# Kernel tuning notes

Measured on AMD Instinct MI355X. Metric: run time of the kernel, lower is better.

Reference implementation:

```python
import jax, jax.numpy as jnp
import numpy as np

N = 50000      # nodes
E = 800000     # edges (avg degree 16)
IN, H, OUT = 128, 128, 64


def setup_inputs() -> dict:
    key = jax.random.key(0)
    k1, k2, k3, k4 = jax.random.split(key, 4)
    x = jax.random.normal(k1, (N, IN), dtype=jnp.float32)
    edge_index = jax.random.randint(k2, (2, E), 0, N, dtype=jnp.int32)
    W1 = jax.random.normal(k3, (IN, H), dtype=jnp.float32) * (1.0 / np.sqrt(IN))
    b1 = jnp.zeros((H,), dtype=jnp.float32)
    W2 = jax.random.normal(k4, (H, OUT), dtype=jnp.float32) * (1.0 / np.sqrt(H))
    b2 = jnp.zeros((OUT,), dtype=jnp.float32)
    return {"x": x, "edge_index": edge_index, "W1": W1, "b1": b1, "W2": W2, "b2": b2}


def gcn_conv(x, edge_index, W, b):
    """PyG GCNConv: D^-1/2 (A + I) D^-1/2 (x W) + b, with self-loops."""
    src, dst = edge_index[0], edge_index[1]
    h = x @ W                                              # [N, F_out] transform first (F_out <= F_in path)
    ones = jnp.ones((src.shape[0],), dtype=h.dtype)
    deg = jax.ops.segment_sum(ones, dst, num_segments=N) + 1.0  # +1 for self-loop
    inv_sqrt_deg = jax.lax.rsqrt(deg)
    norm = inv_sqrt_deg[src] * inv_sqrt_deg[dst]           # [E]
    agg = jax.ops.segment_sum(h[src] * norm[:, None], dst, num_segments=N)
    # self-loop contribution: norm_ii = deg_i^-1
    return agg + h * (1.0 / deg)[:, None] + b


def reference(x, edge_index, W1, b1, W2, b2):
    h = jax.nn.relu(gcn_conv(x, edge_index, W1, b1))
    return gcn_conv(h, edge_index, W2, b2)
```

## Files before the change

kernel.cpp:

```cpp
#include <hip/hip_runtime.h>
#include <hip/hip_bf16.h>


#define GCN_IN   128
#define GCN_H    128
#define GCN_OUT  64
#define CAP      64
#define OVF_CAP  65536
#define SCAT_BLOCKS 2048

using short8 = __attribute__((ext_vector_type(8))) short;
using f32x4  = __attribute__((ext_vector_type(4))) float;
using int4v  = __attribute__((ext_vector_type(4))) int;

__device__ __forceinline__ ushort f2bf(float f) {
    uint b = __float_as_uint(f);
    b = (b + 0x7FFFu + ((b >> 16) & 1u)) >> 16;
    return (ushort)b;
}
__device__ __forceinline__ float bf2f_lo(uint u) { return __uint_as_float(u << 16); }
__device__ __forceinline__ float bf2f_hi(uint u) { return __uint_as_float(u & 0xFFFF0000u); }

__global__ __launch_bounds__(256) void k_fused1(
        const int* __restrict__ src, const int* __restrict__ dst,
        int* __restrict__ cnt, ushort* __restrict__ slot,
        int* __restrict__ ovfcnt, int2* __restrict__ ovf, int E,
        const float* __restrict__ A, const float* __restrict__ B,
        ushort* __restrict__ C, int M, int N) {
    __shared__ __align__(16) ushort As[64][40];
    __shared__ __align__(16) ushort Bs[128][40];
    const int tid = threadIdx.x;

    if (blockIdx.x < SCAT_BLOCKS) {
        const int part = blockIdx.x & 7;
        const int psz  = (N + 7) >> 3;
        const int lo   = part * psz;
        const int hi   = min(lo + psz, N);
        const int bip  = blockIdx.x >> 3;
        const int stride4 = (SCAT_BLOCKS >> 3) * 256 * 4;
        for (int e = (bip * 256 + tid) * 4; e < E; e += stride4) {
            int4v d4 = __builtin_nontemporal_load((const int4v*)(dst + e));
            int4v s4 = __builtin_nontemporal_load((const int4v*)(src + e));
            #pragma unroll
            for (int k = 0; k < 4; ++k) {
                int d = d4[k];
                int s = s4[k];
                if (d >= lo && d < hi) {
                    int pos = atomicAdd(&cnt[d], 1);
                    if (pos < CAP) {
                        slot[(size_t)d * CAP + pos] = (ushort)s;
                    } else {
                        int q = atomicAdd(ovfcnt, 1);
                        if (q < OVF_CAP) ovf[q] = make_int2(d, s);
                    }
                }
            }
        }
        return;
    }

    const int g    = blockIdx.x - SCAT_BLOCKS;
    const int row0 = g * 64;
    const int w    = tid >> 6;
    const int lane = tid & 63;
    const int l15  = lane & 15;
    const int q8   = (lane >> 4) * 8;

    f32x4 acc[8];
    #pragma unroll
    for (int t = 0; t < 8; ++t) {
        acc[t][0] = 0.f; acc[t][1] = 0.f; acc[t][2] = 0.f; acc[t][3] = 0.f;
    }
    for (int kb = 0; kb < 128; kb += 32) {
        #pragma unroll
        for (int tt = 0; tt < 2; ++tt) {
            int f = tid * 4 + tt * 1024;
            int r = f >> 5;
            int k = f & 31;
            float4 v = make_float4(0.f, 0.f, 0.f, 0.f);
            int gr = row0 + r;
            if (gr < M) v = *(const float4*)(A + (size_t)gr * 128 + kb + k);
            ushort4 o;
            o.x = f2bf(v.x); o.y = f2bf(v.y); o.z = f2bf(v.z); o.w = f2bf(v.w);
            *(ushort4*)&As[r][k] = o;
        }
        #pragma unroll
        for (int tt = 0; tt < 4; ++tt) {
            int f = tid * 4 + tt * 1024;
            int k = f >> 7;
            int n = f & 127;
            float4 v = *(const float4*)(B + (size_t)(kb + k) * 128 + n);
            Bs[n + 0][k] = f2bf(v.x);
            Bs[n + 1][k] = f2bf(v.y);
            Bs[n + 2][k] = f2bf(v.z);
            Bs[n + 3][k] = f2bf(v.w);
        }
        __syncthreads();
        short8 a = *(const short8*)&As[16 * w + l15][q8];
        #pragma unroll
        for (int t = 0; t < 8; ++t) {
            short8 b = *(const short8*)&Bs[16 * t + l15][q8];
            acc[t] = __builtin_amdgcn_mfma_f32_16x16x32_bf16(a, b, acc[t], 0, 0, 0);
        }
        __syncthreads();
    }
    const int quad = lane >> 4;
    #pragma unroll
    for (int r = 0; r < 4; ++r) {
        int grow = row0 + 16 * w + quad * 4 + r;
        if (grow < M) {
            #pragma unroll
            for (int t = 0; t < 8; ++t) {
                __builtin_nontemporal_store(
                    f2bf(acc[t][r]), C + (size_t)grow * 128 + 16 * t + l15);
            }
        }
    }
}

__global__ __launch_bounds__(256) void k_agg128(const ushort* __restrict__ h,
                                                const int* __restrict__ cnt,
                                                const ushort* __restrict__ slot,
                                                const float* __restrict__ bias,
                                                const int* __restrict__ ovfcnt,
                                                const int2* __restrict__ ovf,
                                                ushort* __restrict__ out, int n) {
    int node = (blockIdx.x * 256 + threadIdx.x) >> 6;
    int lane = threadIdx.x & 63;
    if (node >= n) return;
    int deg = cnt[node];
    int degm = min(deg, CAP);
    float isd_i = rsqrtf((float)(deg + 1));
    int sidx = (int)__builtin_nontemporal_load(slot + (size_t)node * CAP + lane);
    bool valid = lane < degm;
    if (!valid) sidx = 0;
    float wl = valid ? rsqrtf((float)(cnt[sidx] + 1)) : 0.f;

    const int q = lane >> 4;
    const int i = lane & 15;
    const ushort* hp = h + 8 * i;

    float acc[8] = {};
    for (int j = 0; j < degm; j += 8) {
        int j0 = j + q;
        int j1 = j + 4 + q;
        int   s0 = __shfl(sidx, j0);
        int   s1 = __shfl(sidx, j1);
        float w0 = __shfl(wl, j0);
        float w1 = __shfl(wl, j1);
        uint4 v0 = *(const uint4*)(hp + (size_t)s0 * 128);
        uint4 v1 = *(const uint4*)(hp + (size_t)s1 * 128);
        acc[0] += w0 * bf2f_lo(v0.x) + w1 * bf2f_lo(v1.x);
        acc[1] += w0 * bf2f_hi(v0.x) + w1 * bf2f_hi(v1.x);
        acc[2] += w0 * bf2f_lo(v0.y) + w1 * bf2f_lo(v1.y);
        acc[3] += w0 * bf2f_hi(v0.y) + w1 * bf2f_hi(v1.y);
        acc[4] += w0 * bf2f_lo(v0.z) + w1 * bf2f_lo(v1.z);
        acc[5] += w0 * bf2f_hi(v0.z) + w1 * bf2f_hi(v1.z);
        acc[6] += w0 * bf2f_lo(v0.w) + w1 * bf2f_lo(v1.w);
        acc[7] += w0 * bf2f_hi(v0.w) + w1 * bf2f_hi(v1.w);
    }
    int ovn = *ovfcnt;
    for (int t = 0; t < ovn; ++t) {
        int2 p = ovf[t];
        if (p.x == node && q == 0) {
            float w0 = rsqrtf((float)(cnt[p.y] + 1));
            uint4 v0 = *(const uint4*)(hp + (size_t)p.y * 128);
            acc[0] += w0 * bf2f_lo(v0.x); acc[1] += w0 * bf2f_hi(v0.x);
            acc[2] += w0 * bf2f_lo(v0.y); acc[3] += w0 * bf2f_hi(v0.y);
            acc[4] += w0 * bf2f_lo(v0.z); acc[5] += w0 * bf2f_hi(v0.z);
            acc[6] += w0 * bf2f_lo(v0.w); acc[7] += w0 * bf2f_hi(v0.w);
        }
    }
    #pragma unroll
    for (int k = 0; k < 8; ++k) {
        acc[k] += __shfl_xor(acc[k], 16);
        acc[k] += __shfl_xor(acc[k], 32);
    }
    if (q == 0) {
        uint4 vs = *(const uint4*)(hp + (size_t)node * 128);
        float4 ba = *(const float4*)(bias + 8 * i);
        float4 bb = *(const float4*)(bias + 8 * i + 4);
        float r0 = fmaxf((acc[0] + isd_i * bf2f_lo(vs.x)) * isd_i + ba.x, 0.f);
        float r1 = fmaxf((acc[1] + isd_i * bf2f_hi(vs.x)) * isd_i + ba.y, 0.f);
        float r2 = fmaxf((acc[2] + isd_i * bf2f_lo(vs.y)) * isd_i + ba.z, 0.f);
        float r3 = fmaxf((acc[3] + isd_i * bf2f_hi(vs.y)) * isd_i + ba.w, 0.f);
        float r4 = fmaxf((acc[4] + isd_i * bf2f_lo(vs.z)) * isd_i + bb.x, 0.f);
        float r5 = fmaxf((acc[5] + isd_i * bf2f_hi(vs.z)) * isd_i + bb.y, 0.f);
        float r6 = fmaxf((acc[6] + isd_i * bf2f_lo(vs.w)) * isd_i + bb.z, 0.f);
        float r7 = fmaxf((acc[7] + isd_i * bf2f_hi(vs.w)) * isd_i + bb.w, 0.f);
        uint4 o;
        o.x = (uint)f2bf(r0) | ((uint)f2bf(r1) << 16);
        o.y = (uint)f2bf(r2) | ((uint)f2bf(r3) << 16);
        o.z = (uint)f2bf(r4) | ((uint)f2bf(r5) << 16);
        o.w = (uint)f2bf(r6) | ((uint)f2bf(r7) << 16);
        *(uint4*)(out + (size_t)node * 128 + 8 * i) = o;
    }
}

__global__ __launch_bounds__(256) void k_gemm2(const ushort* __restrict__ A,
                                               const float* __restrict__ B,
                                               const int* __restrict__ cnt,
                                               ushort* __restrict__ C, int M) {
    __shared__ __align__(16) ushort As[64][136];
    __shared__ __align__(16) ushort Bs[64][136];
    const int tid  = threadIdx.x;
    const int w    = tid >> 6;
    const int lane = tid & 63;
    const int l15  = lane & 15;
    const int q8   = (lane >> 4) * 8;
    const int row0 = blockIdx.x * 64;

    #pragma unroll
    for (int t = 0; t < 4; ++t) {
        int f = tid * 8 + t * 2048;
        int r = f >> 7;
        int k = f & 127;
        uint4 v = make_uint4(0u, 0u, 0u, 0u);
        int gr = row0 + r;
        if (gr < M) v = *(const uint4*)(A + (size_t)gr * 128 + k);
        *(uint4*)&As[r][k] = v;
    }
    #pragma unroll
    for (int t = 0; t < 8; ++t) {
        int f = tid * 4 + t * 1024;
        int k = f >> 6;
        int n = f & 63;
        float4 v = *(const float4*)(B + (size_t)k * 64 + n);
        Bs[n + 0][k] = f2bf(v.x);
        Bs[n + 1][k] = f2bf(v.y);
        Bs[n + 2][k] = f2bf(v.z);
        Bs[n + 3][k] = f2bf(v.w);
    }
    __syncthreads();

    f32x4 acc[4];
    #pragma unroll
    for (int t = 0; t < 4; ++t) {
        acc[t][0] = 0.f; acc[t][1] = 0.f; acc[t][2] = 0.f; acc[t][3] = 0.f;
    }
    #pragma unroll
    for (int kt = 0; kt < 4; ++kt) {
        short8 a = *(const short8*)&As[16 * w + l15][32 * kt + q8];
        #pragma unroll
        for (int t = 0; t < 4; ++t) {
            short8 b = *(const short8*)&Bs[16 * t + l15][32 * kt + q8];
            acc[t] = __builtin_amdgcn_mfma_f32_16x16x32_bf16(a, b, acc[t], 0, 0, 0);
        }
    }
    const int quad = lane >> 4;
    #pragma unroll
    for (int r = 0; r < 4; ++r) {
        int grow = row0 + 16 * w + quad * 4 + r;
        if (grow < M) {
            float ws = rsqrtf((float)(cnt[grow] + 1));
            #pragma unroll
            for (int t = 0; t < 4; ++t) {
                C[(size_t)grow * 64 + 16 * t + l15] = f2bf(ws * acc[t][r]);
            }
        }
    }
}

__global__ __launch_bounds__(256) void k_agg64(const ushort* __restrict__ h,
                                               const int* __restrict__ cnt,
                                               const ushort* __restrict__ slot,
                                               const float* __restrict__ bias,
                                               const int* __restrict__ ovfcnt,
                                               const int2* __restrict__ ovf,
                                               float* __restrict__ out, int n) {
    int node = (blockIdx.x * 256 + threadIdx.x) >> 6;
    int lane = threadIdx.x & 63;
    if (node >= n) return;
    int deg = cnt[node];
    int degm = min(deg, CAP);
    float isd_i = rsqrtf((float)(deg + 1));
    int sidx = (int)__builtin_nontemporal_load(slot + (size_t)node * CAP + lane);

    const int g = lane >> 3;
    const int i = lane & 7;
    const ushort* hp = h + 8 * i;

    float acc[8] = {};
    for (int j = 0; j < degm; j += 16) {
        int j0 = j + g;
        int j1 = j + 8 + g;
        int   s0 = __shfl(sidx, j0);
        int   s1 = __shfl(sidx, j1);
        float w0 = (j0 < degm) ? 1.f : 0.f;
        float w1 = (j1 < degm) ? 1.f : 0.f;
        uint4 v0 = *(const uint4*)(hp + (size_t)s0 * 64);
        uint4 v1 = *(const uint4*)(hp + (size_t)s1 * 64);
        acc[0] += w0 * bf2f_lo(v0.x) + w1 * bf2f_lo(v1.x);
        acc[1] += w0 * bf2f_hi(v0.x) + w1 * bf2f_hi(v1.x);
        acc[2] += w0 * bf2f_lo(v0.y) + w1 * bf2f_lo(v1.y);
        acc[3] += w0 * bf2f_hi(v0.y) + w1 * bf2f_hi(v1.y);
        acc[4] += w0 * bf2f_lo(v0.z) + w1 * bf2f_lo(v1.z);
        acc[5] += w0 * bf2f_hi(v0.z) + w1 * bf2f_hi(v1.z);
        acc[6] += w0 * bf2f_lo(v0.w) + w1 * bf2f_lo(v1.w);
        acc[7] += w0 * bf2f_hi(v0.w) + w1 * bf2f_hi(v1.w);
    }
    int ovn = *ovfcnt;
    for (int t = 0; t < ovn; ++t) {
        int2 p = ovf[t];
        if (p.x == node && g == 0) {
            uint4 v0 = *(const uint4*)(hp + (size_t)p.y * 64);
            acc[0] += bf2f_lo(v0.x); acc[1] += bf2f_hi(v0.x);
            acc[2] += bf2f_lo(v0.y); acc[3] += bf2f_hi(v0.y);
            acc[4] += bf2f_lo(v0.z); acc[5] += bf2f_hi(v0.z);
            acc[6] += bf2f_lo(v0.w); acc[7] += bf2f_hi(v0.w);
        }
    }
    #pragma unroll
    for (int k = 0; k < 8; ++k) {
        acc[k] += __shfl_xor(acc[k], 8);
        acc[k] += __shfl_xor(acc[k], 16);
        acc[k] += __shfl_xor(acc[k], 32);
    }
    if (g == 0) {
        uint4 vs = *(const uint4*)(hp + (size_t)node * 64);
        float4 ba = *(const float4*)(bias + 8 * i);
        float4 bb = *(const float4*)(bias + 8 * i + 4);
        float4 r0, r1;
        r0.x = (acc[0] + bf2f_lo(vs.x)) * isd_i + ba.x;
        r0.y = (acc[1] + bf2f_hi(vs.x)) * isd_i + ba.y;
        r0.z = (acc[2] + bf2f_lo(vs.y)) * isd_i + ba.z;
        r0.w = (acc[3] + bf2f_hi(vs.y)) * isd_i + ba.w;
        r1.x = (acc[4] + bf2f_lo(vs.z)) * isd_i + bb.x;
        r1.y = (acc[5] + bf2f_hi(vs.z)) * isd_i + bb.y;
        r1.z = (acc[6] + bf2f_lo(vs.w)) * isd_i + bb.z;
        r1.w = (acc[7] + bf2f_hi(vs.w)) * isd_i + bb.w;
        float* op = out + (size_t)node * 64 + 8 * i;
        *(float4*)op = r0;
        *(float4*)(op + 4) = r1;
    }
}

static inline size_t align256(size_t x) { return (x + 255) & ~(size_t)255; }

extern "C" void kernel_launch(void* const* d_in, const int* in_sizes, int n_in,
                              void* d_out, int out_size, void* d_ws, size_t ws_size,
                              hipStream_t stream) {
    const float* x  = (const float*)d_in[0];
    const int*   ei = (const int*)d_in[1];
    const float* W1 = (const float*)d_in[2];
    const float* b1 = (const float*)d_in[3];
    const float* W2 = (const float*)d_in[4];
    const float* b2 = (const float*)d_in[5];
    float* out = (float*)d_out;

    const int N = in_sizes[0] / GCN_IN;
    const int E = in_sizes[1] / 2;
    const int* src = ei;
    const int* dst = ei + E;

    char* ws = (char*)d_ws;
    size_t o = 0;
    int*    cnt    = (int*)(ws + o);     o += align256((size_t)N * 4);
    int*    ovfcnt = (int*)(ws + o);     o += 256;
    int2*   ovf    = (int2*)(ws + o);    o += align256((size_t)OVF_CAP * 8);
    ushort* slot   = (ushort*)(ws + o);  o += align256((size_t)N * CAP * 2);
    ushort* hb     = (ushort*)(ws + o);  o += align256((size_t)N * GCN_H * 2);
    ushort* h1b    = (ushort*)(ws + o);  o += align256((size_t)N * GCN_H * 2);
    ushort* h2b    = (ushort*)(ws + o);  o += align256((size_t)N * GCN_OUT * 2);

    (void)hipMemsetAsync(cnt, 0, align256((size_t)N * 4) + 256, stream);

    {
        int gemm_blocks = (N + 63) / 64;
        k_fused1<<<SCAT_BLOCKS + gemm_blocks, 256, 0, stream>>>(
            src, dst, cnt, slot, ovfcnt, ovf, E, x, W1, hb, N, N);
    }

    k_agg128<<<(N * 64 + 255) / 256, 256, 0, stream>>>(hb, cnt, slot, b1,
                                                       ovfcnt, ovf, h1b, N);

    k_gemm2<<<(N + 63) / 64, 256, 0, stream>>>(h1b, W2, cnt, h2b, N);

    k_agg64<<<(N * 64 + 255) / 256, 256, 0, stream>>>(h2b, cnt, slot, b2,
                                                      ovfcnt, ovf, out, N);
}
```

Before: 200.4 us.

## Replace global-atomic edge scatter with two-pass bucketed CSR build

The single-pass scatter, where every edge did a global atomicAdd on a per-node counter, is split into two passes. Pass A bins edges into 128-node buckets using LDS atomics and writes them into per-block segments, spilling to a global buffer when a segment fills. Pass B builds each bucket's slot list with shared-memory counters. This removes contended global atomics and the 8x redundant reads of the edge list, at the cost of an extra kernel launch, an intermediate buffer that shares memory with h1b, and a spill path whose scan is repeated by every bucket block.

```diff
diff --git a/kernel.cpp b/kernel.cpp
--- a/kernel.cpp
+++ b/kernel.cpp
@@ -6,8 +6,11 @@
 #define GCN_H    128
 #define GCN_OUT  64
 #define CAP      64
-#define OVF_CAP  65536
-#define SCAT_BLOCKS 2048
+#define OVF_CAP  32768
+#define SPILL_CAP 65536
+#define PASSA_BLOCKS 256
+#define SEG_CAP  24
+#define MAXBUCK  512
 
 using short8 = __attribute__((ext_vector_type(8))) short;
 using f32x4  = __attribute__((ext_vector_type(4))) float;
@@ -23,43 +26,46 @@
 
 __global__ __launch_bounds__(256) void k_fused1(
         const int* __restrict__ src, const int* __restrict__ dst,
-        int* __restrict__ cnt, ushort* __restrict__ slot,
-        int* __restrict__ ovfcnt, int2* __restrict__ ovf, int E,
+        uint* __restrict__ seg, ushort* __restrict__ cntAB,
+        int* __restrict__ spillcnt, uint* __restrict__ spill, int E,
         const float* __restrict__ A, const float* __restrict__ B,
         ushort* __restrict__ C, int M, int N) {
     __shared__ __align__(16) ushort As[64][40];
     __shared__ __align__(16) ushort Bs[128][40];
+    __shared__ int cntL[MAXBUCK];
     const int tid = threadIdx.x;
-
-    if (blockIdx.x < SCAT_BLOCKS) {
-        const int part = blockIdx.x & 7;
-        const int psz  = (N + 7) >> 3;
-        const int lo   = part * psz;
-        const int hi   = min(lo + psz, N);
-        const int bip  = blockIdx.x >> 3;
-        const int stride4 = (SCAT_BLOCKS >> 3) * 256 * 4;
-        for (int e = (bip * 256 + tid) * 4; e < E; e += stride4) {
+    const int nb  = (N + 127) >> 7;
+
+    if (blockIdx.x < PASSA_BLOCKS) {
+        const int blk = blockIdx.x;
+        for (int i = tid; i < nb; i += 256) cntL[i] = 0;
+        __syncthreads();
+        const int stride4 = PASSA_BLOCKS * 256 * 4;
+        for (int e = (blk * 256 + tid) * 4; e < E; e += stride4) {
             int4v d4 = __builtin_nontemporal_load((const int4v*)(dst + e));
             int4v s4 = __builtin_nontemporal_load((const int4v*)(src + e));
             #pragma unroll
             for (int k = 0; k < 4; ++k) {
                 int d = d4[k];
                 int s = s4[k];
-                if (d >= lo && d < hi) {
-                    int pos = atomicAdd(&cnt[d], 1);
-                    if (pos < CAP) {
-                        slot[(size_t)d * CAP + pos] = (ushort)s;
-                    } else {
-                        int q = atomicAdd(ovfcnt, 1);
-                        if (q < OVF_CAP) ovf[q] = make_int2(d, s);
-                    }
+                int b = d >> 7;
+                int pos = atomicAdd(&cntL[b], 1);
+                if (pos < SEG_CAP) {
+                    seg[((size_t)b * PASSA_BLOCKS + blk) * SEG_CAP + pos] =
+                        ((uint)d << 16) | (uint)s;
+                } else {
+                    int q = atomicAdd(spillcnt, 1);
+                    if (q < SPILL_CAP) spill[q] = ((uint)d << 16) | (uint)s;
                 }
             }
         }
+        __syncthreads();
+        for (int b = tid; b < nb; b += 256)
+            cntAB[(size_t)b * PASSA_BLOCKS + blk] = (ushort)min(cntL[b], SEG_CAP);
         return;
     }
 
-    const int g    = blockIdx.x - SCAT_BLOCKS;
+    const int g    = blockIdx.x - PASSA_BLOCKS;
     const int row0 = g * 64;
     const int w    = tid >> 6;
     const int lane = tid & 63;
@@ -114,6 +120,69 @@
                 __builtin_nontemporal_store(
                     f2bf(acc[t][r]), C + (size_t)grow * 128 + 16 * t + l15);
             }
+        }
+    }
+}
+
+__global__ __launch_bounds__(256) void k_passB(const uint* __restrict__ seg,
+                                               const ushort* __restrict__ cntAB,
+                                               const int* __restrict__ spillcnt,
+                                               const uint* __restrict__ spill,
+                                               int* __restrict__ cnt,
+                                               ushort* __restrict__ slot,
+                                               int* __restrict__ ovfcnt,
+                                               int2* __restrict__ ovf, int N) {
+    __shared__ int cntL[128];
+    const int tid  = threadIdx.x;
+    const int b    = blockIdx.x;
+    const int base = b << 7;
+    if (tid < 128) cntL[tid] = 0;
+    __syncthreads();
+
+    const int cs = (int)cntAB[(size_t)b * PASSA_BLOCKS + tid];
+    const uint* sp = seg + ((size_t)b * PASSA_BLOCKS + tid) * SEG_CAP;
+    for (int c4 = 0; c4 < SEG_CAP; c4 += 4) {
+        if (c4 >= cs) break;
+        uint4 v = *(const uint4*)(sp + c4);
+        const uint* vv = (const uint*)&v;
+        #pragma unroll
+        for (int k = 0; k < 4; ++k) {
+            int idx = c4 + k;
+            if (idx < cs) {
+                uint pr = vv[k];
+                int d = (int)(pr >> 16);
+                int s = (int)(pr & 0xFFFFu);
+                int pos = atomicAdd(&cntL[d - base], 1);
+                if (pos < CAP) {
+                    slot[(size_t)d * CAP + pos] = (ushort)s;
+                } else {
+                    int q = atomicAdd(ovfcnt, 1);
+                    if (q < OVF_CAP) ovf[q] = make_int2(d, s);
+                }
+            }
+        }
+    }
+    const int spn = min(*spillcnt, SPILL_CAP);
+    for (int t = tid; t < spn; t += 256) {
+        uint pr = spill[t];
+        int d = (int)(pr >> 16);
+        if (d >= base && d < base + 128) {
+            int s = (int)(pr & 0xFFFFu);
+            int pos = atomicAdd(&cntL[d - base], 1);
+            if (pos < CAP) {
+                slot[(size_t)d * CAP + pos] = (ushort)s;
+            } else {
+                int q = atomicAdd(ovfcnt, 1);
+                if (q < OVF_CAP) ovf[q] = make_int2(d, s);
+            }
+        }
+    }
+    __syncthreads();
+    if (tid < 128) {
+        int d = base + tid;
+        if (d < N) {
+            int c = cntL[tid];
+            if (c) cnt[d] += c;
         }
     }
 }
@@ -336,6 +405,7 @@
 }
 
 static inline size_t align256(size_t x) { return (x + 255) & ~(size_t)255; }
+static inline size_t maxsz(size_t a, size_t b) { return a > b ? a : b; }
 
 extern "C" void kernel_launch(void* const* d_in, const int* in_sizes, int n_in,
                               void* d_out, int out_size, void* d_ws, size_t ws_size,
@@ -352,24 +422,36 @@
     const int E = in_sizes[1] / 2;
     const int* src = ei;
     const int* dst = ei + E;
+    const int nb = (N + 127) >> 7;
 
     char* ws = (char*)d_ws;
     size_t o = 0;
-    int*    cnt    = (int*)(ws + o);     o += align256((size_t)N * 4);
-    int*    ovfcnt = (int*)(ws + o);     o += 256;
-    int2*   ovf    = (int2*)(ws + o);    o += align256((size_t)OVF_CAP * 8);
-    ushort* slot   = (ushort*)(ws + o);  o += align256((size_t)N * CAP * 2);
-    ushort* hb     = (ushort*)(ws + o);  o += align256((size_t)N * GCN_H * 2);
-    ushort* h1b    = (ushort*)(ws + o);  o += align256((size_t)N * GCN_H * 2);
+    int*    cnt     = (int*)(ws + o);    o += align256((size_t)N * 4);
+    int*    ovfcnt  = (int*)(ws + o);
+    int*    spillcnt = ovfcnt + 1;       o += 256;
+    int2*   ovf     = (int2*)(ws + o);   o += align256((size_t)OVF_CAP * 8);
+    uint*   spill   = (uint*)(ws + o);   o += align256((size_t)SPILL_CAP * 4);
+    ushort* slot    = (ushort*)(ws + o); o += align256((size_t)N * CAP * 2);
+    ushort* hb      = (ushort*)(ws + o); o += align256((size_t)N * GCN_H * 2);
+    size_t seg_sz   = align256((size_t)nb * PASSA_BLOCKS * SEG_CAP * 4);
+    size_t cntab_sz = align256((size_t)nb * PASSA_BLOCKS * 2);
+    size_t h1_sz    = align256((size_t)N * GCN_H * 2);
+    char*  zone     = ws + o;            o += maxsz(seg_sz + cntab_sz, h1_sz);
+    uint*   seg    = (uint*)zone;
+    ushort* cntAB  = (ushort*)(zone + seg_sz);
+    ushort* h1b    = (ushort*)zone;
     ushort* h2b    = (ushort*)(ws + o);  o += align256((size_t)N * GCN_OUT * 2);
 
     (void)hipMemsetAsync(cnt, 0, align256((size_t)N * 4) + 256, stream);
 
     {
         int gemm_blocks = (N + 63) / 64;
-        k_fused1<<<SCAT_BLOCKS + gemm_blocks, 256, 0, stream>>>(
-            src, dst, cnt, slot, ovfcnt, ovf, E, x, W1, hb, N, N);
-    }
+        k_fused1<<<PASSA_BLOCKS + gemm_blocks, 256, 0, stream>>>(
+            src, dst, seg, cntAB, spillcnt, spill, E, x, W1, hb, N, N);
+    }
+
+    k_passB<<<nb, 256, 0, stream>>>(seg, cntAB, spillcnt, spill, cnt, slot,
+                                    ovfcnt, ovf, N);
 
     k_agg128<<<(N * 64 + 255) / 256, 256, 0, stream>>>(hb, cnt, slot, b1,
                                                        ovfcnt, ovf, h1b, N);
```

After: 176.4 us. -12.0%, faster.
